# Performance work log

Measured on AMD Instinct MI355X. Metric: run time of the kernel, lower is better.

The kernel has to match this reference:

```python
import jax, jax.numpy as jnp
import numpy as np

N_NODES = 100000
N_EDGES = 1600000
C_IN, C_HID, C_OUT = 64, 64, 32


def _gcn_conv(x, src, dst, ew, W, b, n_nodes):
    """PyG GCNConv: add self-loops (weight 1), symmetric normalization,
    out[dst] += norm * (x @ W)[src], plus bias. Dropout omitted (eval mode)."""
    h = x @ W  # [N, C_out_layer]
    loop = jnp.arange(n_nodes, dtype=src.dtype)
    src_a = jnp.concatenate([src, loop])
    dst_a = jnp.concatenate([dst, loop])
    ew_a = jnp.concatenate([ew, jnp.ones((n_nodes,), dtype=ew.dtype)])
    # degree over incoming (dst) side, weighted
    deg = jax.ops.segment_sum(ew_a, dst_a, num_segments=n_nodes)
    dinv = jnp.where(deg > 0, jax.lax.rsqrt(deg), 0.0)
    norm = dinv[src_a] * ew_a * dinv[dst_a]  # [E+N]
    msg = h[src_a] * norm[:, None]           # gather + scale: [E+N, C]
    out = jax.ops.segment_sum(msg, dst_a, num_segments=n_nodes)  # scatter-add
    return out + b


def setup_inputs() -> dict:
    key = jax.random.key(0)
    k1, k2, k3, k4, k5, k6, k7 = jax.random.split(key, 7)
    x = jax.random.normal(k1, (N_NODES, C_IN), dtype=jnp.float32)
    edge_index = jax.random.randint(k2, (2, N_EDGES), 0, N_NODES, dtype=jnp.int64)
    edge_attr = jax.random.uniform(k3, (N_EDGES,), dtype=jnp.float32)
    s1 = 1.0 / np.sqrt(C_IN)
    s2 = 1.0 / np.sqrt(C_HID)
    W1 = jax.random.uniform(k4, (C_IN, C_HID), jnp.float32, -s1, s1)
    b1 = jnp.zeros((C_HID,), dtype=jnp.float32)
    W2 = jax.random.uniform(k5, (C_HID, C_OUT), jnp.float32, -s2, s2)
    b2 = jnp.zeros((C_OUT,), dtype=jnp.float32)
    return {"x": x, "edge_index": edge_index, "edge_attr": edge_attr,
            "W1": W1, "b1": b1, "W2": W2, "b2": b2}


def reference(x, edge_index, edge_attr, W1, b1, W2, b2):
    n = x.shape[0]
    src, dst = edge_index[0], edge_index[1]
    h = _gcn_conv(x, src, dst, edge_attr, W1, b1, n)
    h = jax.nn.relu(h)  # dropout is identity in eval mode
    out = _gcn_conv(h, src, dst, edge_attr, W2, b2, n)
    return out
```

## Files before the change

kernel.cpp:

```cpp
#include <hip/hip_runtime.h>
#include <hip/hip_fp16.h>


#define TPB 256
#define TPB_P 512
#define TPB_S 1024
#define BSH2 9
#define BN2 512
#define NBC 256
#define PCHUNK 4096
#define CAP2 10752
#define XSTR 68

typedef union { uint2 u; __half2 h[2]; } hpack;
typedef union { uint4 u; __half2 h[4]; } hpack8;

__device__ __forceinline__ int enc_w(float w) {
  unsigned b = __float_as_uint(w);
  return (int)(((b + 0x7FFFu + ((b >> 16) & 1u)) >> 16) & 0x7FFFu);
}
__device__ __forceinline__ float dec_w(int e) {
  return __uint_as_float(((unsigned)e >> 17) << 16);
}

__global__ __launch_bounds__(TPB_P) void k_part(const int* __restrict__ si,
                                                const int* __restrict__ di,
                                                const float* __restrict__ ew,
                                                int* __restrict__ bpos,
                                                int2* __restrict__ tin, int e) {
  __shared__ int hcnt[NBC];
  __shared__ int lst0[NBC];
  __shared__ int lcur[NBC];
  __shared__ int hbase[NBC];
  __shared__ int2 se[PCHUNK];
  __shared__ unsigned char sbk[PCHUNK];
  int t = threadIdx.x;
  int lo = blockIdx.x * PCHUNK;
  int hi = lo + PCHUNK; if (hi > e) hi = e;
  int cn = hi - lo;
  if (t < NBC) hcnt[t] = 0;
  __syncthreads();
  for (int i = lo + t; i < hi; i += TPB_P) atomicAdd(&hcnt[di[i] >> BSH2], 1);
  __syncthreads();
  int c = (t < NBC) ? hcnt[t] : 0;
  for (int off = 1; off < NBC; off <<= 1) {
    int u = (t >= off && t < NBC) ? hcnt[t - off] : 0;
    __syncthreads();
    if (t < NBC) hcnt[t] += u;
    __syncthreads();
  }
  if (t < NBC) {
    int ex = hcnt[t] - c;
    lst0[t] = ex;
    lcur[t] = 0;
    hbase[t] = c ? (t * CAP2 + atomicAdd(&bpos[t], c)) : 0;
  }
  __syncthreads();
  for (int i = lo + t; i < hi; i += TPB_P) {
    int d = di[i];
    int bk = d >> BSH2;
    int loc = atomicAdd(&lcur[bk], 1);
    int p = lst0[bk] + loc;
    se[p] = make_int2(si[i] | ((d & (BN2 - 1)) << 17), __float_as_int(ew[i]));
    sbk[p] = (unsigned char)bk;
  }
  __syncthreads();
  for (int p = t; p < cn; p += TPB_P) {
    int bk = sbk[p];
    tin[hbase[bk] + (p - lst0[bk])] = se[p];
  }
}

__global__ __launch_bounds__(TPB_S) void k_sortb(const int2* __restrict__ tin,
                                                 const int* __restrict__ bpos,
                                                 int* __restrict__ colpk,
                                                 int2* __restrict__ rowseg,
                                                 float* __restrict__ dinv, int n) {
  __shared__ int cnt[BN2];
  __shared__ float degw[BN2];
  __shared__ int cur[BN2];
  __shared__ int ls[BN2];
  int b = blockIdx.x, t = threadIdx.x;
  if (t < BN2) { cnt[t] = 0; degw[t] = 1.0f; }
  __syncthreads();
  int jb = b * CAP2, je = jb + bpos[b];
  for (int j = jb + t; j < je; j += TPB_S) {
    int2 p = tin[j];
    int dl = p.x >> 17;
    atomicAdd(&cnt[dl], 1);
    atomicAdd(&degw[dl], __int_as_float(p.y));
  }
  __syncthreads();
  int c = (t < BN2) ? cnt[t] : 0;
  int c4 = (c + 3) & ~3;
  if (t < BN2) ls[t] = c4;
  __syncthreads();
  for (int off = 1; off < BN2; off <<= 1) {
    int u = (t >= off && t < BN2) ? ls[t - off] : 0;
    __syncthreads();
    if (t < BN2) ls[t] += u;
    __syncthreads();
  }
  int base = b << BSH2;
  if (t < BN2) {
    int start = jb + ls[t] - c4;
    cur[t] = start;
    int node = base + t;
    if (node < n) {
      rowseg[node] = make_int2(start, start + c4);
      dinv[node] = rsqrtf(degw[t]);
    }
    for (int i = c; i < c4; ++i) colpk[start + i] = 0;
  }
  __syncthreads();
  for (int j = jb + t; j < je; j += TPB_S) {
    int2 p = tin[j];
    int dl = p.x >> 17;
    int pos = atomicAdd(&cur[dl], 1);
    colpk[pos] = (p.x & 0x1FFFF) | (enc_w(__int_as_float(p.y)) << 17);
  }
}

__global__ __launch_bounds__(TPB) void k_gemm1(const float* __restrict__ x,
                                               const float* __restrict__ W1,
                                               const float* __restrict__ dinv,
                                               __half* __restrict__ g1h, int n) {
  __shared__ float Wl[64 * 64];
  int t = threadIdx.x;
  {
    const float4* W4 = (const float4*)W1;
    float4* Wl4 = (float4*)Wl;
#pragma unroll
    for (int i = 0; i < 4; ++i) Wl4[t + TPB * i] = W4[t + TPB * i];
  }
  __syncthreads();
  int r = blockIdx.x * 16 + (t >> 4);
  if (r >= n) return;
  int c0 = (t & 15) << 2;
  const float4* xr = (const float4*)(x + (size_t)r * 64);
  float ax = 0.f, ay = 0.f, az = 0.f, aw = 0.f;
#pragma unroll
  for (int kk = 0; kk < 16; ++kk) {
    float4 xv = xr[kk];
    const float* w = &Wl[(kk * 4) * 64 + c0];
    float4 w0 = *(const float4*)(w);
    float4 w1 = *(const float4*)(w + 64);
    float4 w2 = *(const float4*)(w + 128);
    float4 w3 = *(const float4*)(w + 192);
    ax += xv.x * w0.x + xv.y * w1.x + xv.z * w2.x + xv.w * w3.x;
    ay += xv.x * w0.y + xv.y * w1.y + xv.z * w2.y + xv.w * w3.y;
    az += xv.x * w0.z + xv.y * w1.z + xv.z * w2.z + xv.w * w3.z;
    aw += xv.x * w0.w + xv.y * w1.w + xv.z * w2.w + xv.w * w3.w;
  }
  float dv = dinv[r];
  hpack pk;
  pk.h[0] = __floats2half2_rn(dv * ax, dv * ay);
  pk.h[1] = __floats2half2_rn(dv * az, dv * aw);
  *(uint2*)(g1h + (size_t)r * 64 + c0) = pk.u;
}

__global__ __launch_bounds__(TPB) void k_gfuse(const __half* __restrict__ g1h,
                                               const int* __restrict__ colpk,
                                               const int2* __restrict__ rowseg,
                                               const float* __restrict__ dinv,
                                               const float* __restrict__ W2,
                                               const float* __restrict__ b1,
                                               __half* __restrict__ g2h, int n) {
  __shared__ float W2l[64 * 32];
  __shared__ float b1l[64];
  __shared__ float x2l[32 * XSTR];
  int t = threadIdx.x;
  {
    const float4* W4 = (const float4*)W2;
    float4* Wl4 = (float4*)W2l;
#pragma unroll
    for (int i = 0; i < 2; ++i) Wl4[t + TPB * i] = W4[t + TPB * i];
    if (t < 64) b1l[t] = b1[t];
  }
  int node = t >> 3;
  int r = blockIdx.x * 32 + node;
  int c0 = (t & 7) << 3;
  bool valid = (r < n);
  float a[8];
  float dv = 0.f;
  if (valid) {
    dv = dinv[r];
    hpack8 s; s.u = *(const uint4*)(g1h + (size_t)r * 64 + c0);
#pragma unroll
    for (int k = 0; k < 4; ++k) {
      float2 f = __half22float2(s.h[k]);
      a[2 * k] = f.x; a[2 * k + 1] = f.y;
    }
    int2 seg = rowseg[r];
    int j = seg.x;
    for (; j + 7 < seg.y; j += 8) {
      int4 qa = *(const int4*)(colpk + j);
      int4 qb = *(const int4*)(colpk + j + 4);
      hpack8 u0; u0.u = *(const uint4*)(g1h + (size_t)(qa.x & 0x1FFFF) * 64 + c0);
      hpack8 u1; u1.u = *(const uint4*)(g1h + (size_t)(qa.y & 0x1FFFF) * 64 + c0);
      hpack8 u2; u2.u = *(const uint4*)(g1h + (size_t)(qa.z & 0x1FFFF) * 64 + c0);
      hpack8 u3; u3.u = *(const uint4*)(g1h + (size_t)(qa.w & 0x1FFFF) * 64 + c0);
      hpack8 u4; u4.u = *(const uint4*)(g1h + (size_t)(qb.x & 0x1FFFF) * 64 + c0);
      hpack8 u5; u5.u = *(const uint4*)(g1h + (size_t)(qb.y & 0x1FFFF) * 64 + c0);
      hpack8 u6; u6.u = *(const uint4*)(g1h + (size_t)(qb.z & 0x1FFFF) * 64 + c0);
      hpack8 u7; u7.u = *(const uint4*)(g1h + (size_t)(qb.w & 0x1FFFF) * 64 + c0);
      float w0 = dec_w(qa.x), w1 = dec_w(qa.y), w2 = dec_w(qa.z), w3 = dec_w(qa.w);
      float w4 = dec_w(qb.x), w5 = dec_w(qb.y), w6 = dec_w(qb.z), w7 = dec_w(qb.w);
#pragma unroll
      for (int k = 0; k < 4; ++k) {
        float2 f;
        f = __half22float2(u0.h[k]); a[2*k] += w0 * f.x; a[2*k+1] += w0 * f.y;
        f = __half22float2(u1.h[k]); a[2*k] += w1 * f.x; a[2*k+1] += w1 * f.y;
        f = __half22float2(u2.h[k]); a[2*k] += w2 * f.x; a[2*k+1] += w2 * f.y;
        f = __half22float2(u3.h[k]); a[2*k] += w3 * f.x; a[2*k+1] += w3 * f.y;
        f = __half22float2(u4.h[k]); a[2*k] += w4 * f.x; a[2*k+1] += w4 * f.y;
        f = __half22float2(u5.h[k]); a[2*k] += w5 * f.x; a[2*k+1] += w5 * f.y;
        f = __half22float2(u6.h[k]); a[2*k] += w6 * f.x; a[2*k+1] += w6 * f.y;
        f = __half22float2(u7.h[k]); a[2*k] += w7 * f.x; a[2*k+1] += w7 * f.y;
      }
    }
    if (j < seg.y) {
      int4 qa = *(const int4*)(colpk + j);
      hpack8 u0; u0.u = *(const uint4*)(g1h + (size_t)(qa.x & 0x1FFFF) * 64 + c0);
      hpack8 u1; u1.u = *(const uint4*)(g1h + (size_t)(qa.y & 0x1FFFF) * 64 + c0);
      hpack8 u2; u2.u = *(const uint4*)(g1h + (size_t)(qa.z & 0x1FFFF) * 64 + c0);
      hpack8 u3; u3.u = *(const uint4*)(g1h + (size_t)(qa.w & 0x1FFFF) * 64 + c0);
      float w0 = dec_w(qa.x), w1 = dec_w(qa.y), w2 = dec_w(qa.z), w3 = dec_w(qa.w);
#pragma unroll
      for (int k = 0; k < 4; ++k) {
        float2 f;
        f = __half22float2(u0.h[k]); a[2*k] += w0 * f.x; a[2*k+1] += w0 * f.y;
        f = __half22float2(u1.h[k]); a[2*k] += w1 * f.x; a[2*k+1] += w1 * f.y;
        f = __half22float2(u2.h[k]); a[2*k] += w2 * f.x; a[2*k+1] += w2 * f.y;
        f = __half22float2(u3.h[k]); a[2*k] += w3 * f.x; a[2*k+1] += w3 * f.y;
      }
    }
    float* xp = x2l + node * XSTR + c0;
#pragma unroll
    for (int k = 0; k < 8; k += 4) {
      float4 v = {fmaxf(dv * a[k + 0] + b1l[c0 + k + 0], 0.f),
                  fmaxf(dv * a[k + 1] + b1l[c0 + k + 1], 0.f),
                  fmaxf(dv * a[k + 2] + b1l[c0 + k + 2], 0.f),
                  fmaxf(dv * a[k + 3] + b1l[c0 + k + 3], 0.f)};
      *(float4*)(xp + k) = v;
    }
  }
  __syncthreads();
  if (!valid) return;
  int oc = (t & 7) << 2;
  const float* xr = x2l + node * XSTR;
  float ax = 0.f, ay = 0.f, az = 0.f, aw = 0.f;
#pragma unroll
  for (int kk = 0; kk < 16; ++kk) {
    float4 xv = *(const float4*)(xr + 4 * kk);
    const float* w = &W2l[(kk * 4) * 32 + oc];
    float4 w0 = *(const float4*)(w);
    float4 w1 = *(const float4*)(w + 32);
    float4 w2 = *(const float4*)(w + 64);
    float4 w3 = *(const float4*)(w + 96);
    ax += xv.x * w0.x + xv.y * w1.x + xv.z * w2.x + xv.w * w3.x;
    ay += xv.x * w0.y + xv.y * w1.y + xv.z * w2.y + xv.w * w3.y;
    az += xv.x * w0.z + xv.y * w1.z + xv.z * w2.z + xv.w * w3.z;
    aw += xv.x * w0.w + xv.y * w1.w + xv.z * w2.w + xv.w * w3.w;
  }
  hpack pk;
  pk.h[0] = __floats2half2_rn(dv * ax, dv * ay);
  pk.h[1] = __floats2half2_rn(dv * az, dv * aw);
  *(uint2*)(g2h + (size_t)r * 32 + oc) = pk.u;
}

__global__ __launch_bounds__(TPB) void k_gather32(const __half* __restrict__ g2h,
                                                  const int* __restrict__ colpk,
                                                  const int2* __restrict__ rowseg,
                                                  const float* __restrict__ dinv,
                                                  const float* __restrict__ b2,
                                                  float* __restrict__ out, int n) {
  int t = threadIdx.x;
  int r = blockIdx.x * 64 + (t >> 2);
  if (r >= n) return;
  int c0 = (t & 3) << 3;
  float a[8];
  {
    hpack8 s; s.u = *(const uint4*)(g2h + (size_t)r * 32 + c0);
#pragma unroll
    for (int k = 0; k < 4; ++k) {
      float2 f = __half22float2(s.h[k]);
      a[2 * k] = f.x; a[2 * k + 1] = f.y;
    }
  }
  int2 seg = rowseg[r];
  int j = seg.x;
  for (; j + 7 < seg.y; j += 8) {
    int4 qa = *(const int4*)(colpk + j);
    int4 qb = *(const int4*)(colpk + j + 4);
    hpack8 u0; u0.u = *(const uint4*)(g2h + (size_t)(qa.x & 0x1FFFF) * 32 + c0);
    hpack8 u1; u1.u = *(const uint4*)(g2h + (size_t)(qa.y & 0x1FFFF) * 32 + c0);
    hpack8 u2; u2.u = *(const uint4*)(g2h + (size_t)(qa.z & 0x1FFFF) * 32 + c0);
    hpack8 u3; u3.u = *(const uint4*)(g2h + (size_t)(qa.w & 0x1FFFF) * 32 + c0);
    hpack8 u4; u4.u = *(const uint4*)(g2h + (size_t)(qb.x & 0x1FFFF) * 32 + c0);
    hpack8 u5; u5.u = *(const uint4*)(g2h + (size_t)(qb.y & 0x1FFFF) * 32 + c0);
    hpack8 u6; u6.u = *(const uint4*)(g2h + (size_t)(qb.z & 0x1FFFF) * 32 + c0);
    hpack8 u7; u7.u = *(const uint4*)(g2h + (size_t)(qb.w & 0x1FFFF) * 32 + c0);
    float w0 = dec_w(qa.x), w1 = dec_w(qa.y), w2 = dec_w(qa.z), w3 = dec_w(qa.w);
    float w4 = dec_w(qb.x), w5 = dec_w(qb.y), w6 = dec_w(qb.z), w7 = dec_w(qb.w);
#pragma unroll
    for (int k = 0; k < 4; ++k) {
      float2 f;
      f = __half22float2(u0.h[k]); a[2*k] += w0 * f.x; a[2*k+1] += w0 * f.y;
      f = __half22float2(u1.h[k]); a[2*k] += w1 * f.x; a[2*k+1] += w1 * f.y;
      f = __half22float2(u2.h[k]); a[2*k] += w2 * f.x; a[2*k+1] += w2 * f.y;
      f = __half22float2(u3.h[k]); a[2*k] += w3 * f.x; a[2*k+1] += w3 * f.y;
      f = __half22float2(u4.h[k]); a[2*k] += w4 * f.x; a[2*k+1] += w4 * f.y;
      f = __half22float2(u5.h[k]); a[2*k] += w5 * f.x; a[2*k+1] += w5 * f.y;
      f = __half22float2(u6.h[k]); a[2*k] += w6 * f.x; a[2*k+1] += w6 * f.y;
      f = __half22float2(u7.h[k]); a[2*k] += w7 * f.x; a[2*k+1] += w7 * f.y;
    }
  }
  if (j < seg.y) {
    int4 qa = *(const int4*)(colpk + j);
    hpack8 u0; u0.u = *(const uint4*)(g2h + (size_t)(qa.x & 0x1FFFF) * 32 + c0);
    hpack8 u1; u1.u = *(const uint4*)(g2h + (size_t)(qa.y & 0x1FFFF) * 32 + c0);
    hpack8 u2; u2.u = *(const uint4*)(g2h + (size_t)(qa.z & 0x1FFFF) * 32 + c0);
    hpack8 u3; u3.u = *(const uint4*)(g2h + (size_t)(qa.w & 0x1FFFF) * 32 + c0);
    float w0 = dec_w(qa.x), w1 = dec_w(qa.y), w2 = dec_w(qa.z), w3 = dec_w(qa.w);
#pragma unroll
    for (int k = 0; k < 4; ++k) {
      float2 f;
      f = __half22float2(u0.h[k]); a[2*k] += w0 * f.x; a[2*k+1] += w0 * f.y;
      f = __half22float2(u1.h[k]); a[2*k] += w1 * f.x; a[2*k+1] += w1 * f.y;
      f = __half22float2(u2.h[k]); a[2*k] += w2 * f.x; a[2*k+1] += w2 * f.y;
      f = __half22float2(u3.h[k]); a[2*k] += w3 * f.x; a[2*k+1] += w3 * f.y;
    }
  }
  float dv = dinv[r];
  const float4* b24 = (const float4*)(b2 + c0);
  float4 bb0 = b24[0], bb1 = b24[1];
  float* op = out + (size_t)r * 32 + c0;
  *(float4*)(op)     = make_float4(dv * a[0] + bb0.x, dv * a[1] + bb0.y,
                                   dv * a[2] + bb0.z, dv * a[3] + bb0.w);
  *(float4*)(op + 4) = make_float4(dv * a[4] + bb1.x, dv * a[5] + bb1.y,
                                   dv * a[6] + bb1.z, dv * a[7] + bb1.w);
}

extern "C" void kernel_launch(void* const* d_in, const int* in_sizes, int n_in,
                              void* d_out, int out_size, void* d_ws, size_t ws_size,
                              hipStream_t stream) {
  const float* x  = (const float*)d_in[0];
  const int* ei   = (const int*)d_in[1];
  const float* ew = (const float*)d_in[2];
  const float* W1 = (const float*)d_in[3];
  const float* b1 = (const float*)d_in[4];
  const float* W2 = (const float*)d_in[5];
  const float* b2 = (const float*)d_in[6];
  float* out = (float*)d_out;

  const int n = in_sizes[0] / 64;
  const int e = in_sizes[1] / 2;
  const int* si = ei;
  const int* di = ei + e;
  const int NBc = (n + BN2 - 1) >> BSH2;

  float* ws = (float*)d_ws;
  const size_t NP = 100352;
  float*  dinv   = ws;
  __half* g1h    = (__half*)(ws + NP);
  int2*   rowseg = (int2*)(ws + NP + (size_t)n * 32);
  int*    bpos   = (int*)(rowseg + NP);
  int*    colpk  = bpos + 1024;
  int2*   tin    = (int2*)(colpk + (size_t)NBC * CAP2);
  __half* g2h    = (__half*)(tin + (size_t)NBC * CAP2);

  int gb_part = (e + PCHUNK - 1) / PCHUNK;
  int gb_g1 = (n + 15) / 16;
  int gb_gf = (n + 31) / 32;
  int gb_g32 = (n + 63) / 64;

  hipMemsetAsync(bpos, 0, NBC * sizeof(int), stream);
  k_part<<<gb_part, TPB_P, 0, stream>>>(si, di, ew, bpos, tin, e);
  k_sortb<<<NBc, TPB_S, 0, stream>>>(tin, bpos, colpk, rowseg, dinv, n);
  k_gemm1<<<gb_g1, TPB, 0, stream>>>(x, W1, dinv, g1h, n);
  k_gfuse<<<gb_gf, TPB, 0, stream>>>(g1h, colpk, rowseg, dinv, W2, b1, g2h, n);
  k_gather32<<<gb_g32, TPB, 0, stream>>>(g2h, colpk, rowseg, dinv, b2, out, n);
}
```

Before: 204.0 us.

## Fuse first-layer GEMM into per-bucket sort kernel

```diff
diff --git a/kernel.cpp b/kernel.cpp
--- a/kernel.cpp
+++ b/kernel.cpp
@@ -75,13 +75,18 @@
                                                  const int* __restrict__ bpos,
                                                  int* __restrict__ colpk,
                                                  int2* __restrict__ rowseg,
-                                                 float* __restrict__ dinv, int n) {
+                                                 float* __restrict__ dinv,
+                                                 const float* __restrict__ x,
+                                                 const float* __restrict__ W1,
+                                                 __half* __restrict__ g1h, int n) {
   __shared__ int cnt[BN2];
   __shared__ float degw[BN2];
   __shared__ int cur[BN2];
   __shared__ int ls[BN2];
+  __shared__ float W1l[64 * 64];
   int b = blockIdx.x, t = threadIdx.x;
   if (t < BN2) { cnt[t] = 0; degw[t] = 1.0f; }
+  ((float4*)W1l)[t] = ((const float4*)W1)[t];
   __syncthreads();
   int jb = b * CAP2, je = jb + bpos[b];
   for (int j = jb + t; j < je; j += TPB_S) {
@@ -119,44 +124,31 @@
     int pos = atomicAdd(&cur[dl], 1);
     colpk[pos] = (p.x & 0x1FFFF) | (enc_w(__int_as_float(p.y)) << 17);
   }
-}
-
-__global__ __launch_bounds__(TPB) void k_gemm1(const float* __restrict__ x,
-                                               const float* __restrict__ W1,
-                                               const float* __restrict__ dinv,
-                                               __half* __restrict__ g1h, int n) {
-  __shared__ float Wl[64 * 64];
-  int t = threadIdx.x;
-  {
-    const float4* W4 = (const float4*)W1;
-    float4* Wl4 = (float4*)Wl;
-#pragma unroll
-    for (int i = 0; i < 4; ++i) Wl4[t + TPB * i] = W4[t + TPB * i];
-  }
-  __syncthreads();
-  int r = blockIdx.x * 16 + (t >> 4);
-  if (r >= n) return;
   int c0 = (t & 15) << 2;
-  const float4* xr = (const float4*)(x + (size_t)r * 64);
-  float ax = 0.f, ay = 0.f, az = 0.f, aw = 0.f;
-#pragma unroll
-  for (int kk = 0; kk < 16; ++kk) {
-    float4 xv = xr[kk];
-    const float* w = &Wl[(kk * 4) * 64 + c0];
-    float4 w0 = *(const float4*)(w);
-    float4 w1 = *(const float4*)(w + 64);
-    float4 w2 = *(const float4*)(w + 128);
-    float4 w3 = *(const float4*)(w + 192);
-    ax += xv.x * w0.x + xv.y * w1.x + xv.z * w2.x + xv.w * w3.x;
-    ay += xv.x * w0.y + xv.y * w1.y + xv.z * w2.y + xv.w * w3.y;
-    az += xv.x * w0.z + xv.y * w1.z + xv.z * w2.z + xv.w * w3.z;
-    aw += xv.x * w0.w + xv.y * w1.w + xv.z * w2.w + xv.w * w3.w;
-  }
-  float dv = dinv[r];
-  hpack pk;
-  pk.h[0] = __floats2half2_rn(dv * ax, dv * ay);
-  pk.h[1] = __floats2half2_rn(dv * az, dv * aw);
-  *(uint2*)(g1h + (size_t)r * 64 + c0) = pk.u;
+  for (int rr = (t >> 4); rr < BN2; rr += 64) {
+    int r = base + rr;
+    if (r >= n) continue;
+    const float4* xr = (const float4*)(x + (size_t)r * 64);
+    float ax = 0.f, ay = 0.f, az = 0.f, aw = 0.f;
+#pragma unroll
+    for (int kk = 0; kk < 16; ++kk) {
+      float4 xv = xr[kk];
+      const float* w = &W1l[(kk * 4) * 64 + c0];
+      float4 w0 = *(const float4*)(w);
+      float4 w1 = *(const float4*)(w + 64);
+      float4 w2 = *(const float4*)(w + 128);
+      float4 w3 = *(const float4*)(w + 192);
+      ax += xv.x * w0.x + xv.y * w1.x + xv.z * w2.x + xv.w * w3.x;
+      ay += xv.x * w0.y + xv.y * w1.y + xv.z * w2.y + xv.w * w3.y;
+      az += xv.x * w0.z + xv.y * w1.z + xv.z * w2.z + xv.w * w3.z;
+      aw += xv.x * w0.w + xv.y * w1.w + xv.z * w2.w + xv.w * w3.w;
+    }
+    float dv = rsqrtf(degw[rr]);
+    hpack pk;
+    pk.h[0] = __floats2half2_rn(dv * ax, dv * ay);
+    pk.h[1] = __floats2half2_rn(dv * az, dv * aw);
+    *(uint2*)(g1h + (size_t)r * 64 + c0) = pk.u;
+  }
 }
 
 __global__ __launch_bounds__(TPB) void k_gfuse(const __half* __restrict__ g1h,
@@ -362,23 +354,23 @@
 
   float* ws = (float*)d_ws;
   const size_t NP = 100352;
+  const size_t SLOTS = (size_t)NBC * CAP2;
   float*  dinv   = ws;
   __half* g1h    = (__half*)(ws + NP);
   int2*   rowseg = (int2*)(ws + NP + (size_t)n * 32);
   int*    bpos   = (int*)(rowseg + NP);
   int*    colpk  = bpos + 1024;
-  int2*   tin    = (int2*)(colpk + (size_t)NBC * CAP2);
-  __half* g2h    = (__half*)(tin + (size_t)NBC * CAP2);
+  int2*   tin    = (int2*)(colpk + SLOTS);
+  __half* g2h    = (__half*)(tin + SLOTS);
 
   int gb_part = (e + PCHUNK - 1) / PCHUNK;
-  int gb_g1 = (n + 15) / 16;
   int gb_gf = (n + 31) / 32;
   int gb_g32 = (n + 63) / 64;
 
   hipMemsetAsync(bpos, 0, NBC * sizeof(int), stream);
   k_part<<<gb_part, TPB_P, 0, stream>>>(si, di, ew, bpos, tin, e);
-  k_sortb<<<NBc, TPB_S, 0, stream>>>(tin, bpos, colpk, rowseg, dinv, n);
-  k_gemm1<<<gb_g1, TPB, 0, stream>>>(x, W1, dinv, g1h, n);
+  k_sortb<<<NBc, TPB_S, 0, stream>>>(tin, bpos, colpk, rowseg, dinv,
+                                     x, W1, g1h, n);
   k_gfuse<<<gb_gf, TPB, 0, stream>>>(g1h, colpk, rowseg, dinv, W2, b1, g2h, n);
   k_gather32<<<gb_g32, TPB, 0, stream>>>(g2h, colpk, rowseg, dinv, b2, out, n);
 }
```

Measured after the change: 207.6 us. No clear change (+1.8%).
